# Performance work log

Measured on AMD Instinct MI355X. Metric: run time of the kernel, lower is better.

## Reference

```python
import jax, jax.numpy as jnp
import numpy as np
import math

E = 1024   # embedding_size
H = 16     # layer_size (num heads)
DK = 64    # key_size
DH = 64    # head_size
HID = 4096 # hidden_size
B = 2
S = 2048   # context_size
EPS = 1e-5


def layer_norm(x, w, b):
    mu = jnp.mean(x, axis=-1, keepdims=True)
    var = jnp.mean(jnp.square(x - mu), axis=-1, keepdims=True)
    return (x - mu) * jax.lax.rsqrt(var + EPS) * w + b


def setup_inputs() -> dict:
    key = jax.random.key(0)
    ks = jax.random.split(key, 16)
    sE = 1.0 / math.sqrt(E)
    sH = 1.0 / math.sqrt(HID)
    return {
        "embeddings": jax.random.normal(ks[0], (B, S, E), dtype=jnp.float32),
        "Wq": jax.random.uniform(ks[1], (H, E, DK), minval=-sE, maxval=sE, dtype=jnp.float32),
        "bq": jnp.zeros((H, DK), dtype=jnp.float32),
        "Wk": jax.random.uniform(ks[2], (H, E, DK), minval=-sE, maxval=sE, dtype=jnp.float32),
        "bk": jnp.zeros((H, DK), dtype=jnp.float32),
        "Wv": jax.random.uniform(ks[3], (H, E, DH), minval=-sE, maxval=sE, dtype=jnp.float32),
        "bv": jnp.zeros((H, DH), dtype=jnp.float32),
        "ln1_w": jnp.ones((E,), dtype=jnp.float32),
        "ln1_b": jnp.zeros((E,), dtype=jnp.float32),
        "ln2_w": jnp.ones((E,), dtype=jnp.float32),
        "ln2_b": jnp.zeros((E,), dtype=jnp.float32),
        "W1": jax.random.uniform(ks[4], (E, HID), minval=-sE, maxval=sE, dtype=jnp.float32),
        "b1": jnp.zeros((HID,), dtype=jnp.float32),
        "W2": jax.random.uniform(ks[5], (HID, E), minval=-sH, maxval=sH, dtype=jnp.float32),
        "b2": jnp.zeros((E,), dtype=jnp.float32),
    }


def reference(embeddings, Wq, bq, Wk, bk, Wv, bv, ln1_w, ln1_b, ln2_w, ln2_b, W1, b1, W2, b2):
    # NOTE: faithful to source: residual uses the POST-norm activations
    # (embeddings is reassigned to the LayerNorm output before the residual add).
    x = layer_norm(embeddings, ln1_w, ln1_b)            # [B,S,E]
    q = jnp.einsum('bse,hed->bhsd', x, Wq) + bq[:, None, :]
    k = jnp.einsum('bse,hed->bhsd', x, Wk) + bk[:, None, :]
    v = jnp.einsum('bse,hed->bhsd', x, Wv) + bv[:, None, :]
    scores = jnp.einsum('bhsd,bhtd->bhst', q, k) / math.sqrt(DK)  # [B,H,S,S]
    causal = jnp.tril(jnp.ones((S, S), dtype=bool))
    scores = jnp.where(causal, scores, -jnp.inf)
    w = jax.nn.softmax(scores, axis=-1)
    o = jnp.einsum('bhst,bhtd->bhsd', w, v)             # [B,H,S,DH]
    o = jnp.transpose(o, (0, 2, 1, 3)).reshape(B, S, H * DH)  # concat heads
    x = x + o
    y = layer_norm(x, ln2_w, ln2_b)
    h = jax.nn.relu(jnp.einsum('bse,eh->bsh', y, W1) + b1)
    out = y + jnp.einsum('bsh,he->bse', h, W2) + b2
    return out
```

## Files before the change

kernel.cpp:

```cpp
#include <hip/hip_runtime.h>


typedef unsigned short u16;
typedef unsigned int   u32;
typedef __bf16 bf16x8 __attribute__((ext_vector_type(8)));
typedef float  f32x4  __attribute__((ext_vector_type(4)));

#define NEG_INF (-__builtin_inff())

__device__ __forceinline__ u16 f2b(float f) {
  u32 u = __float_as_uint(f);
  u = (u + 0x7fffu + ((u >> 16) & 1u)) >> 16;
  return (u16)u;
}

__device__ __forceinline__ void gload16(const void* g, void* l) {
  __builtin_amdgcn_global_load_lds(
      (const __attribute__((address_space(1))) u32*)g,
      (__attribute__((address_space(3))) u32*)l, 16, 0, 0);
}

__global__ __launch_bounds__(256)
void transpose_bf16_k(const float* __restrict__ in, u16* __restrict__ out,
                      int R, int C) {
  __shared__ float tile[64][65];
  int r0 = blockIdx.x * 64, c0 = blockIdx.y * 64;
  const float* ip = in + (size_t)blockIdx.z * R * C;
  u16* op = out + (size_t)blockIdx.z * C * R;
  int tr = threadIdx.x >> 6, tc = threadIdx.x & 63;
#pragma unroll
  for (int i = 0; i < 16; i++) {
    int r = i * 4 + tr;
    tile[r][tc] = ip[(size_t)(r0 + r) * C + c0 + tc];
  }
  __syncthreads();
#pragma unroll
  for (int i = 0; i < 16; i++) {
    int c = i * 4 + tr;
    op[(size_t)(c0 + c) * R + r0 + tc] = f2b(tile[tc][c]);
  }
}

__global__ __launch_bounds__(256)
void vtrans_k(const u16* __restrict__ vin, u16* __restrict__ vt) {
  __shared__ __align__(16) u16 tile[64][72];
  int s0 = blockIdx.x * 64, bh = blockIdx.y;
  const u16* ip = vin + (size_t)bh * 2048 * 64;
  u16* op = vt + (size_t)bh * 64 * 2048;
  int t = threadIdx.x;
#pragma unroll
  for (int i = 0; i < 2; i++) {
    int idx = i * 256 + t, r = idx >> 3, c = idx & 7;
    *(uint4*)&tile[r][c * 8] = *(const uint4*)(ip + (size_t)(s0 + r) * 64 + c * 8);
  }
  __syncthreads();
#pragma unroll
  for (int i = 0; i < 16; i++) {
    int d = i * 4 + (t >> 6), s = t & 63;
    op[(size_t)d * 2048 + s0 + s] = tile[s][d];
  }
}

__global__ __launch_bounds__(256)
void ln_k(const float* __restrict__ in, const float* __restrict__ in2,
          const float* __restrict__ w, const float* __restrict__ b,
          float* __restrict__ outf, u16* __restrict__ outb) {
  int row = blockIdx.x, t = threadIdx.x;
  const float4* ip = (const float4*)(in + (size_t)row * 1024);
  float4 x = ip[t];
  if (in2) {
    const float4* ip2 = (const float4*)(in2 + (size_t)row * 1024);
    float4 o = ip2[t];
    x.x += o.x; x.y += o.y; x.z += o.z; x.w += o.w;
  }
  float s = x.x + x.y + x.z + x.w;
  float q = x.x * x.x + x.y * x.y + x.z * x.z + x.w * x.w;
#pragma unroll
  for (int m = 32; m; m >>= 1) { s += __shfl_xor(s, m); q += __shfl_xor(q, m); }
  __shared__ float rs[4], rq[4];
  if ((t & 63) == 0) { rs[t >> 6] = s; rq[t >> 6] = q; }
  __syncthreads();
  s = rs[0] + rs[1] + rs[2] + rs[3];
  q = rq[0] + rq[1] + rq[2] + rq[3];
  float mean = s * (1.f / 1024.f);
  float var  = q * (1.f / 1024.f) - mean * mean;
  float rstd = rsqrtf(var + 1e-5f);
  float4 wv = ((const float4*)w)[t];
  float4 bv = ((const float4*)b)[t];
  float4 y;
  y.x = (x.x - mean) * rstd * wv.x + bv.x;
  y.y = (x.y - mean) * rstd * wv.y + bv.y;
  y.z = (x.z - mean) * rstd * wv.z + bv.z;
  y.w = (x.w - mean) * rstd * wv.w + bv.w;
  if (outf) ((float4*)(outf + (size_t)row * 1024))[t] = y;
  ushort4 ub;
  ub.x = f2b(y.x); ub.y = f2b(y.y); ub.z = f2b(y.z); ub.w = f2b(y.w);
  ((ushort4*)(outb + (size_t)row * 1024))[t] = ub;
}

#define EPI_QKV  0
#define EPI_RELU 1
#define EPI_RES  2

template <int EPI>
__global__ __launch_bounds__(256)
void gemm_k(const u16* __restrict__ A, const u16* __restrict__ Bt,
            int K, int lda, int ldbt,
            const float* __restrict__ bias0, const float* __restrict__ bias1,
            const float* __restrict__ bias2, const float* __restrict__ res,
            int ldout, u16* __restrict__ outb, float* __restrict__ outf) {
  __shared__ __align__(16) u16 As[128 * 32];
  __shared__ __align__(16) u16 Bs[128 * 32];
  int t = threadIdx.x;
  int wave = t >> 6, lane = t & 63, quad = lane >> 4, l16 = lane & 15;
  int wm = (wave >> 1) * 64, wn = (wave & 1) * 64;
  int bm = blockIdx.x * 128, bn = blockIdx.y * 128;

  const u16* Ag = A + (size_t)(bm + (t >> 2)) * lda + (t & 3) * 8;
  const u16* Bg = Bt + (size_t)(bn + (t >> 2)) * ldbt + (t & 3) * 8;
  u16* Asl = As + t * 8;
  u16* Bsl = Bs + t * 8;

  f32x4 acc[4][4] = {};

  for (int k0 = 0; k0 < K; k0 += 32) {
    gload16(Ag + k0, Asl);
    gload16(Ag + k0 + (size_t)64 * lda, Asl + 2048);
    gload16(Bg + k0, Bsl);
    gload16(Bg + k0 + (size_t)64 * ldbt, Bsl + 2048);
    __syncthreads();
    bf16x8 af[4], bfr[4];
#pragma unroll
    for (int i = 0; i < 4; i++)
      af[i] = *(const bf16x8*)(As + (wm + i * 16 + l16) * 32 + quad * 8);
#pragma unroll
    for (int j = 0; j < 4; j++)
      bfr[j] = *(const bf16x8*)(Bs + (wn + j * 16 + l16) * 32 + quad * 8);
#pragma unroll
    for (int i = 0; i < 4; i++)
#pragma unroll
      for (int j = 0; j < 4; j++)
        acc[i][j] = __builtin_amdgcn_mfma_f32_16x16x32_bf16(af[i], bfr[j],
                                                            acc[i][j], 0, 0, 0);
    __syncthreads();
  }

#pragma unroll
  for (int i = 0; i < 4; i++) {
#pragma unroll
    for (int j = 0; j < 4; j++) {
      int c = bn + wn + j * 16 + l16;
#pragma unroll
      for (int rr = 0; rr < 4; rr++) {
        int r = bm + wm + i * 16 + quad * 4 + rr;
        float v = acc[i][j][rr];
        if (EPI == EPI_QKV) {
          int which = c >> 10, h = (c >> 6) & 15, d = c & 63;
          const float* bp = which == 0 ? bias0 : (which == 1 ? bias1 : bias2);
          v += bp[h * 64 + d];
          int bb = r >> 11, ss = r & 2047;
          outb[((size_t)(which * 32 + bb * 16 + h) * 2048 + ss) * 64 + d] = f2b(v);
        } else if (EPI == EPI_RELU) {
          v += bias0[c];
          v = v > 0.f ? v : 0.f;
          outb[(size_t)r * ldout + c] = f2b(v);
        } else {
          v += bias0[c] + res[(size_t)r * ldout + c];
          outf[(size_t)r * ldout + c] = v;
        }
      }
    }
  }
}

__global__ __launch_bounds__(512, 4)
void attn_k(const u16* __restrict__ qkv, const u16* __restrict__ vt,
            float* __restrict__ o) {
  int bh = blockIdx.y;
  int Qt = (bh >> 4) ? (15 - (int)blockIdx.x) : (int)blockIdx.x;
  int b = bh >> 4, h = bh & 15;
  const u16* qg = qkv + (size_t)bh * (2048 * 64) + (size_t)Qt * 128 * 64;
  const u16* kg = qkv + (size_t)(32 + bh) * (2048 * 64);
  const u16* vg = vt + (size_t)bh * (64 * 2048);

  __shared__ __align__(16) u16 Qs[128 * 64];
  __shared__ __align__(16) u16 Ks[2][64 * 64];
  __shared__ __align__(16) u16 Vs[2][64 * 64];
  __shared__ __align__(16) u16 Ps[8][16 * 64];

  int t = threadIdx.x;
  int wave = t >> 6, lane = t & 63, quad = lane >> 4, l16 = lane & 15;

  {
#pragma unroll
    for (int i = 0; i < 2; i++) {
      int idx = i * 512 + t, r = idx >> 3, c = (idx & 7) ^ (r & 7);
      gload16(qg + r * 64 + c * 8, Qs + idx * 8);
    }
    int r = t >> 3, c = (t & 7) ^ (r & 7);
    gload16(kg + (size_t)r * 64 + c * 8, Ks[0] + t * 8);
    gload16(vg + (size_t)r * 2048 + c * 8, Vs[0] + t * 8);
  }
  __syncthreads();

  int x7 = l16 & 7;
  bf16x8 qf[2];
  {
    const u16* qr = Qs + (wave * 16 + l16) * 64;
    qf[0] = *(const bf16x8*)(qr + ((quad ^ x7) * 8));
    qf[1] = *(const bf16x8*)(qr + (((4 + quad) ^ x7) * 8));
  }

  f32x4 oacc[4] = {};
  float mo[4] = {NEG_INF, NEG_INF, NEG_INF, NEG_INF};
  float ll[4] = {};
  u16* Pw = Ps[wave];
  int rmin = Qt * 128 + wave * 16;
  int kmax_w = (rmin + 15) >> 6;
  int klast = 2 * Qt + 1;

  for (int kt = 0; kt <= klast; kt++) {
    const u16* ks = Ks[kt & 1];
    const u16* vs = Vs[kt & 1];
    if (kt < klast) {
      int r = t >> 3, c = (t & 7) ^ (r & 7);
      gload16(kg + (size_t)((kt + 1) * 64 + r) * 64 + c * 8, Ks[(kt + 1) & 1] + t * 8);
      gload16(vg + (size_t)r * 2048 + (kt + 1) * 64 + c * 8, Vs[(kt + 1) & 1] + t * 8);
    }
    if (kt <= kmax_w) {
      f32x4 sc[4];
#pragma unroll
      for (int g = 0; g < 4; g++) {
        const u16* kr = ks + (g * 16 + l16) * 64;
        bf16x8 kf0 = *(const bf16x8*)(kr + ((quad ^ x7) * 8));
        bf16x8 kf1 = *(const bf16x8*)(kr + (((4 + quad) ^ x7) * 8));
        f32x4 s = {};
        s = __builtin_amdgcn_mfma_f32_16x16x32_bf16(qf[0], kf0, s, 0, 0, 0);
        s = __builtin_amdgcn_mfma_f32_16x16x32_bf16(qf[1], kf1, s, 0, 0, 0);
        sc[g] = s;
      }
      if (kt * 64 + 63 > rmin) {
#pragma unroll
        for (int g = 0; g < 4; g++) {
          int col = kt * 64 + g * 16 + l16;
#pragma unroll
          for (int rr = 0; rr < 4; rr++) {
            int row = rmin + quad * 4 + rr;
            sc[g][rr] = (col <= row) ? sc[g][rr] * 0.125f : NEG_INF;
          }
        }
      } else {
#pragma unroll
        for (int g = 0; g < 4; g++)
#pragma unroll
          for (int rr = 0; rr < 4; rr++) sc[g][rr] *= 0.125f;
      }
      float al[4], rsum[4];
#pragma unroll
      for (int rr = 0; rr < 4; rr++) {
        float mx = fmaxf(fmaxf(sc[0][rr], sc[1][rr]), fmaxf(sc[2][rr], sc[3][rr]));
        mx = fmaxf(mx, __shfl_xor(mx, 1));
        mx = fmaxf(mx, __shfl_xor(mx, 2));
        mx = fmaxf(mx, __shfl_xor(mx, 4));
        mx = fmaxf(mx, __shfl_xor(mx, 8));
        float mnew = fmaxf(mo[rr], mx);
        al[rr] = __expf(mo[rr] - mnew);
        mo[rr] = mnew;
        rsum[rr] = 0.f;
      }
#pragma unroll
      for (int g = 0; g < 4; g++) {
        int cbase = (g * 16 + l16 + quad * 16) & 63;
#pragma unroll
        for (int rr = 0; rr < 4; rr++) {
          float p = __expf(sc[g][rr] - mo[rr]);
          rsum[rr] += p;
          Pw[(quad * 4 + rr) * 64 + cbase] = f2b(p);
        }
      }
#pragma unroll
      for (int rr = 0; rr < 4; rr++) {
        rsum[rr] += __shfl_xor(rsum[rr], 1);
        rsum[rr] += __shfl_xor(rsum[rr], 2);
        rsum[rr] += __shfl_xor(rsum[rr], 4);
        rsum[rr] += __shfl_xor(rsum[rr], 8);
        ll[rr] = ll[rr] * al[rr] + rsum[rr];
      }
#pragma unroll
      for (int g = 0; g < 4; g++)
#pragma unroll
        for (int rr = 0; rr < 4; rr++) oacc[g][rr] *= al[rr];
      bf16x8 pf0, pf1;
      {
        const u16* pr = Pw + l16 * 64;
        int sh = (l16 & 12) * 4;
        pf0 = *(const bf16x8*)(pr + ((quad * 8 + sh) & 63));
        pf1 = *(const bf16x8*)(pr + ((32 + quad * 8 + sh) & 63));
      }
#pragma unroll
      for (int g = 0; g < 4; g++) {
        const u16* vr = vs + (g * 16 + l16) * 64;
        bf16x8 vf0 = *(const bf16x8*)(vr + ((quad ^ x7) * 8));
        bf16x8 vf1 = *(const bf16x8*)(vr + (((4 + quad) ^ x7) * 8));
        oacc[g] = __builtin_amdgcn_mfma_f32_16x16x32_bf16(pf0, vf0, oacc[g], 0, 0, 0);
        oacc[g] = __builtin_amdgcn_mfma_f32_16x16x32_bf16(pf1, vf1, oacc[g], 0, 0, 0);
      }
    }
    __syncthreads();
  }

#pragma unroll
  for (int g = 0; g < 4; g++)
#pragma unroll
    for (int rr = 0; rr < 4; rr++) {
      int srow = rmin + quad * 4 + rr;
      o[((size_t)b * 2048 + srow) * 1024 + h * 64 + g * 16 + l16] =
          oacc[g][rr] / ll[rr];
    }
}

extern "C" void kernel_launch(void* const* d_in, const int* in_sizes, int n_in,
                              void* d_out, int out_size, void* d_ws, size_t ws_size,
                              hipStream_t stream) {
  const float* emb  = (const float*)d_in[0];
  const float* Wq   = (const float*)d_in[1];
  const float* bq   = (const float*)d_in[2];
  const float* Wk   = (const float*)d_in[3];
  const float* bk   = (const float*)d_in[4];
  const float* Wv   = (const float*)d_in[5];
  const float* bv   = (const float*)d_in[6];
  const float* ln1w = (const float*)d_in[7];
  const float* ln1b = (const float*)d_in[8];
  const float* ln2w = (const float*)d_in[9];
  const float* ln2b = (const float*)d_in[10];
  const float* W1   = (const float*)d_in[11];
  const float* b1   = (const float*)d_in[12];
  const float* W2   = (const float*)d_in[13];
  const float* b2   = (const float*)d_in[14];
  float* out = (float*)d_out;

  char* p = (char*)d_ws;
  u16*   Wqkv_t = (u16*)p;   p += (size_t)3072 * 1024 * 2;
  u16*   W1t    = (u16*)p;   p += (size_t)4096 * 1024 * 2;
  u16*   W2t    = (u16*)p;   p += (size_t)1024 * 4096 * 2;
  float* x      = (float*)p; p += (size_t)4096 * 1024 * 4;
  u16*   xb     = (u16*)p;   p += (size_t)4096 * 1024 * 2;
  u16*   qkvb   = (u16*)p;   p += (size_t)3 * 32 * 2048 * 64 * 2;
  float* ob     = (float*)p; p += (size_t)4096 * 1024 * 4;
  float* y      = (float*)p; p += (size_t)4096 * 1024 * 4;
  u16*   yb     = (u16*)p;   p += (size_t)4096 * 1024 * 2;
  u16*   hb     = (u16*)qkvb;
  u16*   vT     = (u16*)y;
  if (ws_size < (size_t)(p - (char*)d_ws)) return;

  transpose_bf16_k<<<dim3(16, 1, 16), 256, 0, stream>>>(Wq, Wqkv_t,                   1024, 64);
  transpose_bf16_k<<<dim3(16, 1, 16), 256, 0, stream>>>(Wk, Wqkv_t + 1024 * 1024,     1024, 64);
  transpose_bf16_k<<<dim3(16, 1, 16), 256, 0, stream>>>(Wv, Wqkv_t + 2 * 1024 * 1024, 1024, 64);
  transpose_bf16_k<<<dim3(16, 64, 1), 256, 0, stream>>>(W1, W1t, 1024, 4096);
  transpose_bf16_k<<<dim3(64, 16, 1), 256, 0, stream>>>(W2, W2t, 4096, 1024);

  ln_k<<<dim3(4096), 256, 0, stream>>>(emb, nullptr, ln1w, ln1b, x, xb);

  gemm_k<EPI_QKV><<<dim3(32, 24), 256, 0, stream>>>(
      xb, Wqkv_t, 1024, 1024, 1024, bq, bk, bv, nullptr, 0, qkvb, nullptr);

  vtrans_k<<<dim3(32, 32), 256, 0, stream>>>(qkvb + (size_t)64 * 2048 * 64, vT);

  attn_k<<<dim3(16, 32), 512, 0, stream>>>(qkvb, vT, ob);

  ln_k<<<dim3(4096), 256, 0, stream>>>(x, ob, ln2w, ln2b, y, yb);

  gemm_k<EPI_RELU><<<dim3(32, 32), 256, 0, stream>>>(
      yb, W1t, 1024, 1024, 1024, b1, nullptr, nullptr, nullptr, 4096, hb, nullptr);

  gemm_k<EPI_RES><<<dim3(32, 8), 256, 0, stream>>>(
      hb, W2t, 4096, 4096, 4096, b2, nullptr, nullptr, y, 1024, nullptr, out);
}
```

Before: 393.9 us.

## Double GEMM K-tile to 64 with XOR-swizzled LDS and split-K the W2 GEMM

```diff
diff --git a/kernel.cpp b/kernel.cpp
--- a/kernel.cpp
+++ b/kernel.cpp
@@ -108,40 +108,57 @@
             int K, int lda, int ldbt,
             const float* __restrict__ bias0, const float* __restrict__ bias1,
             const float* __restrict__ bias2, const float* __restrict__ res,
-            int ldout, u16* __restrict__ outb, float* __restrict__ outf) {
-  __shared__ __align__(16) u16 As[128 * 32];
-  __shared__ __align__(16) u16 Bs[128 * 32];
+            int ldout, u16* __restrict__ outb, float* __restrict__ outf,
+            float* __restrict__ outp) {
+  __shared__ __align__(16) u16 As[128 * 64];
+  __shared__ __align__(16) u16 Bs[128 * 64];
   int t = threadIdx.x;
   int wave = t >> 6, lane = t & 63, quad = lane >> 4, l16 = lane & 15;
+  int x7 = l16 & 7;
   int wm = (wave >> 1) * 64, wn = (wave & 1) * 64;
   int bm = blockIdx.x * 128, bn = blockIdx.y * 128;
-
-  const u16* Ag = A + (size_t)(bm + (t >> 2)) * lda + (t & 3) * 8;
-  const u16* Bg = Bt + (size_t)(bn + (t >> 2)) * ldbt + (t & 3) * 8;
+  int zoff = blockIdx.z * K;
+
+  const u16* Agl[4];
+  const u16* Bgl[4];
+#pragma unroll
+  for (int i = 0; i < 4; i++) {
+    int idx = i * 256 + t, r = idx >> 3, c = (idx & 7) ^ (r & 7);
+    Agl[i] = A + (size_t)(bm + r) * lda + zoff + c * 8;
+    Bgl[i] = Bt + (size_t)(bn + r) * ldbt + zoff + c * 8;
+  }
   u16* Asl = As + t * 8;
   u16* Bsl = Bs + t * 8;
 
   f32x4 acc[4][4] = {};
 
-  for (int k0 = 0; k0 < K; k0 += 32) {
-    gload16(Ag + k0, Asl);
-    gload16(Ag + k0 + (size_t)64 * lda, Asl + 2048);
-    gload16(Bg + k0, Bsl);
-    gload16(Bg + k0 + (size_t)64 * ldbt, Bsl + 2048);
+  for (int k0 = 0; k0 < K; k0 += 64) {
+#pragma unroll
+    for (int i = 0; i < 4; i++) {
+      gload16(Agl[i] + k0, Asl + i * 2048);
+      gload16(Bgl[i] + k0, Bsl + i * 2048);
+    }
     __syncthreads();
-    bf16x8 af[4], bfr[4];
-#pragma unroll
-    for (int i = 0; i < 4; i++)
-      af[i] = *(const bf16x8*)(As + (wm + i * 16 + l16) * 32 + quad * 8);
-#pragma unroll
-    for (int j = 0; j < 4; j++)
-      bfr[j] = *(const bf16x8*)(Bs + (wn + j * 16 + l16) * 32 + quad * 8);
-#pragma unroll
-    for (int i = 0; i < 4; i++)
-#pragma unroll
-      for (int j = 0; j < 4; j++)
-        acc[i][j] = __builtin_amdgcn_mfma_f32_16x16x32_bf16(af[i], bfr[j],
-                                                            acc[i][j], 0, 0, 0);
+#pragma unroll
+    for (int kc = 0; kc < 2; kc++) {
+      bf16x8 af[4], bfr[4];
+#pragma unroll
+      for (int i = 0; i < 4; i++) {
+        int r = wm + i * 16 + l16;
+        af[i] = *(const bf16x8*)(As + r * 64 + (((kc * 4 + quad) ^ x7) * 8));
+      }
+#pragma unroll
+      for (int j = 0; j < 4; j++) {
+        int r = wn + j * 16 + l16;
+        bfr[j] = *(const bf16x8*)(Bs + r * 64 + (((kc * 4 + quad) ^ x7) * 8));
+      }
+#pragma unroll
+      for (int i = 0; i < 4; i++)
+#pragma unroll
+        for (int j = 0; j < 4; j++)
+          acc[i][j] = __builtin_amdgcn_mfma_f32_16x16x32_bf16(af[i], bfr[j],
+                                                              acc[i][j], 0, 0, 0);
+    }
     __syncthreads();
   }
 
@@ -165,12 +182,25 @@
           v = v > 0.f ? v : 0.f;
           outb[(size_t)r * ldout + c] = f2b(v);
         } else {
-          v += bias0[c] + res[(size_t)r * ldout + c];
-          outf[(size_t)r * ldout + c] = v;
+          if (blockIdx.z == 0) {
+            v += bias0[c] + res[(size_t)r * ldout + c];
+            outf[(size_t)r * ldout + c] = v;
+          } else {
+            outp[(size_t)r * ldout + c] = v;
+          }
         }
       }
     }
   }
+}
+
+__global__ __launch_bounds__(256)
+void reduce_k(float* __restrict__ out, const float* __restrict__ part) {
+  int i = blockIdx.x * 256 + threadIdx.x;
+  float4 a = ((const float4*)part)[i];
+  float4 b = ((float4*)out)[i];
+  b.x += a.x; b.y += a.y; b.z += a.z; b.w += a.w;
+  ((float4*)out)[i] = b;
 }
 
 __global__ __launch_bounds__(512, 4)
@@ -351,6 +381,7 @@
   u16*   yb     = (u16*)p;   p += (size_t)4096 * 1024 * 2;
   u16*   hb     = (u16*)qkvb;
   u16*   vT     = (u16*)y;
+  float* part   = x;
   if (ws_size < (size_t)(p - (char*)d_ws)) return;
 
   transpose_bf16_k<<<dim3(16, 1, 16), 256, 0, stream>>>(Wq, Wqkv_t,                   1024, 64);
@@ -361,8 +392,8 @@
 
   ln_k<<<dim3(4096), 256, 0, stream>>>(emb, nullptr, ln1w, ln1b, x, xb);
 
-  gemm_k<EPI_QKV><<<dim3(32, 24), 256, 0, stream>>>(
-      xb, Wqkv_t, 1024, 1024, 1024, bq, bk, bv, nullptr, 0, qkvb, nullptr);
+  gemm_k<EPI_QKV><<<dim3(32, 24, 1), 256, 0, stream>>>(
+      xb, Wqkv_t, 1024, 1024, 1024, bq, bk, bv, nullptr, 0, qkvb, nullptr, nullptr);
 
   vtrans_k<<<dim3(32, 32), 256, 0, stream>>>(qkvb + (size_t)64 * 2048 * 64, vT);
 
@@ -370,9 +401,11 @@
 
   ln_k<<<dim3(4096), 256, 0, stream>>>(x, ob, ln2w, ln2b, y, yb);
 
-  gemm_k<EPI_RELU><<<dim3(32, 32), 256, 0, stream>>>(
-      yb, W1t, 1024, 1024, 1024, b1, nullptr, nullptr, nullptr, 4096, hb, nullptr);
-
-  gemm_k<EPI_RES><<<dim3(32, 8), 256, 0, stream>>>(
-      hb, W2t, 4096, 4096, 4096, b2, nullptr, nullptr, y, 1024, nullptr, out);
-}
+  gemm_k<EPI_RELU><<<dim3(32, 32, 1), 256, 0, stream>>>(
+      yb, W1t, 1024, 1024, 1024, b1, nullptr, nullptr, nullptr, 4096, hb, nullptr, nullptr);
+
+  gemm_k<EPI_RES><<<dim3(32, 8, 2), 256, 0, stream>>>(
+      hb, W2t, 2048, 4096, 4096, b2, nullptr, nullptr, y, 1024, nullptr, out, part);
+
+  reduce_k<<<dim3(4096), 256, 0, stream>>>(out, part);
+}
```

Result: faster. 359.4 us (-8.8%).
